# Kernel optimization log

Hardware: AMD Instinct MI355X
Metric: run time of the kernel (lower is better)

The kernel has to match this reference:

```python
import jax, jax.numpy as jnp
import numpy as np

LN_EPS = 1e-5

def _layernorm(z, g, b):
    m = jnp.mean(z, axis=-1, keepdims=True)
    v = jnp.mean(jnp.square(z - m), axis=-1, keepdims=True)
    return (z - m) / jnp.sqrt(v + LN_EPS) * g + b

def setup_inputs() -> dict:
    key = jax.random.key(0)
    ks = jax.random.split(key, 8)
    B, N, C, H = 16, 1024, 384, 6
    Dff = 4 * C
    s = 0.02
    return {
        "x": jax.random.normal(ks[0], (B, N, C), dtype=jnp.float32),
        "ln1_g": jnp.ones((C,), jnp.float32),
        "ln1_b": jnp.zeros((C,), jnp.float32),
        "qkv_w": jax.random.normal(ks[1], (3 * C, C), jnp.float32) * s,
        "proj_w": jax.random.normal(ks[2], (C, C), jnp.float32) * s,
        "proj_b": jnp.zeros((C,), jnp.float32),
        "gate_h": jnp.ones((H,), jnp.float32),
        "ln2_g": jnp.ones((C,), jnp.float32),
        "ln2_b": jnp.zeros((C,), jnp.float32),
        "fc1_w": jax.random.normal(ks[3], (Dff, C), jnp.float32) * s,
        "fc1_b": jnp.zeros((Dff,), jnp.float32),
        "fc2_w": jax.random.normal(ks[4], (C, Dff), jnp.float32) * s,
        "fc2_b": jnp.zeros((C,), jnp.float32),
        "gate_mlp": jnp.ones((Dff,), jnp.float32),
    }

def reference(x, ln1_g, ln1_b, qkv_w, proj_w, proj_b, gate_h,
              ln2_g, ln2_b, fc1_w, fc1_b, fc2_w, fc2_b, gate_mlp):
    B, N, C = x.shape
    H = gate_h.shape[0]
    Dh = C // H
    scale = Dh ** -0.5

    # Attention branch
    h = _layernorm(x, ln1_g, ln1_b)
    qkv = (h @ qkv_w.T).reshape(B, N, 3, H, Dh).transpose(2, 0, 3, 1, 4)  # [3,B,H,N,Dh]
    q, k, v = qkv[0], qkv[1], qkv[2]
    attn = jax.nn.softmax(jnp.einsum('bhnd,bhmd->bhnm', q, k) * scale, axis=-1)  # [B,H,N,N]
    o = jnp.einsum('bhnm,bhmd->bhnd', attn, v)            # [B,H,N,Dh]
    o = o.transpose(0, 2, 1, 3) * gate_h[None, None, :, None]  # per-head gate
    o = o.reshape(B, N, C) @ proj_w.T + proj_b
    x = x + o

    # MLP branch (exact GELU, per-neuron gate)
    h2 = _layernorm(x, ln2_g, ln2_b)
    m = jax.nn.gelu(h2 @ fc1_w.T + fc1_b, approximate=False) * gate_mlp
    x = x + (m @ fc2_w.T + fc2_b)
    return x
```

## Files before the change

kernel.cpp:

```cpp
#include <hip/hip_runtime.h>
#include <hip/hip_bf16.h>
#include <cstdint>
#include <cstddef>

#define B_   16
#define N_   1024
#define C_   384
#define H_   6
#define DFF_ 1536
#define R_   16384

typedef __attribute__((ext_vector_type(8))) __bf16 bf16x8;
typedef __attribute__((ext_vector_type(4))) float  f32x4;
typedef __attribute__((ext_vector_type(8))) unsigned short u16x8;
typedef __attribute__((ext_vector_type(4))) unsigned short u16x4;

__device__ __forceinline__ float bf2f(unsigned short u){
    unsigned int x = ((unsigned int)u) << 16;
    return __builtin_bit_cast(float, x);
}
__device__ __forceinline__ unsigned short f2bf(float f){
    return __builtin_bit_cast(unsigned short, __float2bfloat16(f));
}
__device__ __forceinline__ unsigned int cvt_pk_bf16(float a, float b){
    unsigned int r;
    asm("v_cvt_pk_bf16_f32 %0, %1, %2" : "=v"(r) : "v"(a), "v"(b));
    return r;
}
__device__ __forceinline__ float fast_exp2(float x){
    float r;
    asm("v_exp_f32 %0, %1" : "=v"(r) : "v"(x));
    return r;
}
__device__ __forceinline__ void gload16(const void* g, void* l){
    __builtin_amdgcn_global_load_lds(
        (const __attribute__((address_space(1))) unsigned int*)g,
        (__attribute__((address_space(3))) unsigned int*)l, 16, 0, 0);
}
__device__ __forceinline__ float gelu_f(float u){
    float z  = fabsf(u) * 0.70710678118654752f;
    float t  = __builtin_amdgcn_rcpf(1.0f + 0.47047f*z);
    float e  = __expf(-z*z);
    float p  = t*(0.3480242f + t*(-0.0958798f + t*0.7478556f));
    float er = 1.0f - p*e;
    return 0.5f*u*(1.0f + copysignf(er, u));
}
__device__ __forceinline__ float ldv(const float* p, size_t i){ return p[i]; }
__device__ __forceinline__ float ldv(const __hip_bfloat16* p, size_t i){ return __bfloat162float(p[i]); }

__global__ __launch_bounds__(256) void ln1_cvt_kernel(
    const float* __restrict__ x, const float* __restrict__ g,
    const float* __restrict__ b, __hip_bfloat16* __restrict__ out,
    const float* __restrict__ i0, __hip_bfloat16* __restrict__ o0, int n0,
    const float* __restrict__ i1, __hip_bfloat16* __restrict__ o1, int n1,
    const float* __restrict__ i2, __hip_bfloat16* __restrict__ o2, int n2,
    const float* __restrict__ i3, __hip_bfloat16* __restrict__ o3, int n3)
{
    if (blockIdx.x < 4096){
        const int lane = threadIdx.x & 63;
        const int wave = threadIdx.x >> 6;
        const int row  = blockIdx.x*4 + wave;
        const float* xr = x + (size_t)row*C_;
        float v[6];
        float s = 0.f;
        #pragma unroll
        for (int i=0;i<6;i++){ v[i] = xr[lane + i*64]; s += v[i]; }
        #pragma unroll
        for (int m=1;m<64;m<<=1) s += __shfl_xor(s, m);
        const float mean = s * (1.0f/C_);
        float sq = 0.f;
        #pragma unroll
        for (int i=0;i<6;i++){ float d = v[i]-mean; sq += d*d; }
        #pragma unroll
        for (int m=1;m<64;m<<=1) sq += __shfl_xor(sq, m);
        const float rstd = rsqrtf(sq*(1.0f/C_) + 1e-5f);
        #pragma unroll
        for (int i=0;i<6;i++){
            int c = lane + i*64;
            out[(size_t)row*C_ + c] = __float2bfloat16((v[i]-mean)*rstd*g[c] + b[c]);
        }
    } else {
        const int total = n0+n1+n2+n3;
        for (int i = (blockIdx.x-4096)*blockDim.x + threadIdx.x; i < total; i += 1024*blockDim.x){
            int k = i;
            if (k < n0){ o0[k] = __float2bfloat16(i0[k]); continue; }
            k -= n0;
            if (k < n1){ o1[k] = __float2bfloat16(i1[k]); continue; }
            k -= n1;
            if (k < n2){ o2[k] = __float2bfloat16(i2[k]); continue; }
            k -= n2;
            o3[k] = __float2bfloat16(i3[k]);
        }
    }
}

template<typename T>
__global__ __launch_bounds__(256) void ln_kernel(
    const T* __restrict__ x, const float* __restrict__ g,
    const float* __restrict__ b, __hip_bfloat16* __restrict__ out)
{
    const int lane = threadIdx.x & 63;
    const int wave = threadIdx.x >> 6;
    const int row  = blockIdx.x*4 + wave;
    const T* xr = x + (size_t)row*C_;
    float v[6];
    float s = 0.f;
    #pragma unroll
    for (int i=0;i<6;i++){ v[i] = ldv(xr, lane + i*64); s += v[i]; }
    #pragma unroll
    for (int m=1;m<64;m<<=1) s += __shfl_xor(s, m);
    const float mean = s * (1.0f/C_);
    float sq = 0.f;
    #pragma unroll
    for (int i=0;i<6;i++){ float d = v[i]-mean; sq += d*d; }
    #pragma unroll
    for (int m=1;m<64;m<<=1) sq += __shfl_xor(sq, m);
    const float rstd = rsqrtf(sq*(1.0f/C_) + 1e-5f);
    #pragma unroll
    for (int i=0;i<6;i++){
        int c = lane + i*64;
        out[(size_t)row*C_ + c] = __float2bfloat16((v[i]-mean)*rstd*g[c] + b[c]);
    }
}

#define BK2 32
enum { EPI_QKV=0, EPI_PROJ=1, EPI_FC1=2, EPI_FC2=3 };

template<int EPI, int BMt, int BNt, int NBUF, int MW, int NTH>
__global__ __launch_bounds__(NTH, MW) void gemm_bt(
    const __hip_bfloat16* __restrict__ A,
    const __hip_bfloat16* __restrict__ W,
    const int M, const int N, const int K,
    const float* __restrict__ bias,
    const float* __restrict__ resid,
    const __hip_bfloat16* __restrict__ residb,
    const float* __restrict__ gate,
    float* __restrict__ outf,
    __hip_bfloat16* __restrict__ outb)
{
    constexpr int NWAVE = NTH/64;
    constexpr int NWC   = (BNt >= 128) ? 2 : 1;
    constexpr int NWR   = NWAVE/NWC;
    constexpr int WRS   = BMt/NWR;
    constexpr int MI    = WRS/16;
    constexpr int APASS = (BMt*BK2*2)/(NTH*16);
    constexpr int BPASS = (BNt*BK2*2)/(NTH*16);
    constexpr int LPT   = APASS + BPASS;
    constexpr int RPP   = NTH/4;
    __shared__ __align__(16) unsigned short As[NBUF][BMt*BK2];
    __shared__ __align__(16) unsigned short Bs[NBUF][BNt*BK2];
    const int t = threadIdx.x;
    const int l = t & 63;
    const int w = t >> 6;
    const int wr = (NWC==2) ? (w >> 1) : w;
    const int wc = (NWC==2) ? (w & 1)  : 0;
    const int nb = N / BNt;
    const int rbX = (M/BMt) >> 3;
    const int X  = blockIdx.x & 7;
    const int j8 = blockIdx.x >> 3;
    const int rb = X*rbX + j8 / nb;
    const int cb = j8 % nb;
    const int srow2 = t >> 2;
    const int sgcol = (((t&3) - ((t>>3)&3)) & 3) * 8;
    f32x4 acc[MI][4];
    #pragma unroll
    for (int i=0;i<MI;i++)
        #pragma unroll
        for (int jj=0;jj<4;jj++) acc[i][jj] = (f32x4){0.f,0.f,0.f,0.f};

    const size_t arow0 = (size_t)rb*BMt + srow2;
    const size_t brow0 = (size_t)cb*BNt + srow2;

    auto STAGE = [&](int buf, int k0){
        #pragma unroll
        for (int c=0;c<APASS;c++)
            gload16(A + (arow0 + c*RPP)*K + k0 + sgcol, (char*)&As[buf][0] + c*(NTH*16) + t*16);
        #pragma unroll
        for (int c=0;c<BPASS;c++)
            gload16(W + (brow0 + c*RPP)*K + k0 + sgcol, (char*)&Bs[buf][0] + c*(NTH*16) + t*16);
    };

    auto COMPUTE = [&](int buf){
        const char* as = (const char*)&As[buf][0];
        const char* bs = (const char*)&Bs[buf][0];
        bf16x8 af[MI], bw[4];
        #pragma unroll
        for (int i=0;i<MI;i++){
            const int r = wr*WRS + i*16 + (l&15);
            const int sl = ((l>>4) + ((r>>1)&3)) & 3;
            af[i] = *(const bf16x8*)(as + r*64 + sl*16);
        }
        #pragma unroll
        for (int i=0;i<4;i++){
            const int r = wc*64 + i*16 + (l&15);
            const int sl = ((l>>4) + ((r>>1)&3)) & 3;
            bw[i] = *(const bf16x8*)(bs + r*64 + sl*16);
        }
        #pragma unroll
        for (int mi=0;mi<MI;mi++)
            #pragma unroll
            for (int ni=0;ni<4;ni++)
                acc[mi][ni] = __builtin_amdgcn_mfma_f32_16x16x32_bf16(af[mi], bw[ni], acc[mi][ni], 0,0,0);
    };

    const int nst = K/BK2;
    if constexpr (NBUF==2){
        STAGE(0, 0);
        for (int s=0; s<nst; ++s){
            asm volatile("s_waitcnt vmcnt(0)" ::: "memory");
            __builtin_amdgcn_s_barrier();
            asm volatile("" ::: "memory");
            if (s+1 < nst) STAGE((s+1)&1, (s+1)*BK2);
            COMPUTE(s&1);
        }
    } else {
        STAGE(0, 0);
        STAGE(1, BK2);
        int cur = 0, stb = 2;
        for (int s=0; s<nst; ++s){
            if (s < nst-1){
                if constexpr (LPT==4) asm volatile("s_waitcnt vmcnt(4)" ::: "memory");
                else                  asm volatile("s_waitcnt vmcnt(3)" ::: "memory");
            } else {
                asm volatile("s_waitcnt vmcnt(0)" ::: "memory");
            }
            __builtin_amdgcn_s_barrier();
            asm volatile("" ::: "memory");
            if (s+2 < nst){
                STAGE(stb, (s+2)*BK2);
                stb = (stb+1==3) ? 0 : stb+1;
            }
            COMPUTE(cur);
            cur = (cur+1==3) ? 0 : cur+1;
        }
    }
    const int rowBase = rb*BMt + wr*WRS;
    const int colBase = cb*BNt + wc*64;
    #pragma unroll
    for (int ni=0; ni<4; ni++){
        const int col = colBase + ni*16 + (l&15);
        #pragma unroll
        for (int mi=0; mi<MI; mi++){
            #pragma unroll
            for (int jj=0;jj<4;jj++){
                const int row = rowBase + mi*16 + (l>>4)*4 + jj;
                const float vx = acc[mi][ni][jj];
                size_t idx = (size_t)row*N + col;
                if constexpr (EPI==EPI_PROJ){
                    outb[idx] = __float2bfloat16(resid[idx] + vx + bias[col]);
                } else if constexpr (EPI==EPI_FC2){
                    outf[idx] = bf2f(*((const unsigned short*)residb + idx)) + vx + bias[col];
                } else {
                    outb[idx] = __float2bfloat16(gelu_f(vx + bias[col]) * gate[col]);
                }
            }
        }
    }
}

template<int EPI, int NCOLS>
__global__ __launch_bounds__(256, 2) void gemm_wres(
    const __hip_bfloat16* __restrict__ A,
    const __hip_bfloat16* __restrict__ Wt,
    const float* __restrict__ bias,
    const float* __restrict__ resid,
    const float* __restrict__ gate,
    __hip_bfloat16* __restrict__ outb)
{
    constexpr int NB = NCOLS/64;
    constexpr int G  = 24;
    __shared__ __align__(16) unsigned short As[4][128*32];
    __shared__ __align__(16) unsigned short Bs[64*384];
    const int t = threadIdx.x;
    const int l = t & 63;
    const int w = t >> 6;
    const int X  = blockIdx.x & 7;
    const int j8 = blockIdx.x >> 3;
    const int rb = X*8 + j8 / NB;
    const int cb = j8 % NB;

    #pragma unroll
    for (int j=0;j<12;j++){
        const int L     = (w*12 + j)*1024 + l*16;
        const int row   = L / 768;
        const int cbyte = L - row*768;
        const int scol  = (cbyte ^ ((row&7)<<4)) >> 1;
        gload16(Wt + (size_t)(cb*64 + row)*384 + scol, (char*)&Bs[0] + L);
    }
    const int sgcol = (((l&3) - ((l>>3)&3)) & 3) * 8;
    const size_t arow0 = (size_t)rb*256 + w*32 + (l>>2);
    auto STAGEA = [&](int g){
        const int rt = g/12, s = g - rt*12;
        #pragma unroll
        for (int c=0;c<2;c++)
            gload16(A + (arow0 + rt*128 + c*16)*384 + s*32 + sgcol,
                    (char*)&As[g&3][0] + w*2048 + c*1024 + l*16);
    };
    STAGEA(0); STAGEA(1); STAGEA(2);
    asm volatile("s_waitcnt vmcnt(6)" ::: "memory");
    __builtin_amdgcn_s_barrier();

    #pragma unroll
    for (int rt=0; rt<2; ++rt){
        f32x4 acc[2][4];
        #pragma unroll
        for (int i=0;i<2;i++)
            #pragma unroll
            for (int jj=0;jj<4;jj++) acc[i][jj] = (f32x4){0.f,0.f,0.f,0.f};

        #pragma unroll
        for (int s=0; s<12; ++s){
            const int g = rt*12 + s;
            if (g <= G-3)      asm volatile("s_waitcnt vmcnt(4)" ::: "memory");
            else if (g == G-2) asm volatile("s_waitcnt vmcnt(2)" ::: "memory");
            else               asm volatile("s_waitcnt vmcnt(0)" ::: "memory");
            const char* as = (const char*)&As[g&3][0] + w*2048;
            bf16x8 af[2], bw[4];
            #pragma unroll
            for (int i=0;i<2;i++){
                const int r  = i*16 + (l&15);
                const int sl = ((l>>4) + ((r>>1)&3)) & 3;
                af[i] = *(const bf16x8*)(as + r*64 + sl*16);
            }
            #pragma unroll
            for (int i=0;i<4;i++){
                const int r = i*16 + (l&15);
                bw[i] = *(const bf16x8*)((const char*)&Bs[0] + r*768
                             + ((s*64 + (l>>4)*16) ^ ((r&7)<<4)));
            }
            #pragma unroll
            for (int mi=0;mi<2;mi++)
                #pragma unroll
                for (int ni=0;ni<4;ni++)
                    acc[mi][ni] = __builtin_amdgcn_mfma_f32_16x16x32_bf16(af[mi], bw[ni], acc[mi][ni], 0,0,0);
            asm volatile("s_waitcnt lgkmcnt(0)" ::: "memory");
            if (g+3 < G) STAGEA(g+3);
        }
        const int rowBase = rb*256 + rt*128 + w*32;
        if constexpr (EPI==EPI_QKV){
            unsigned short* ob = (unsigned short*)outb;
            #pragma unroll
            for (int ni=0; ni<4; ni++){
                const int col = cb*64 + ni*16 + (l&15);
                const int p = col/384, rem = col - p*384;
                const int hh = rem>>6, d = rem&63;
                #pragma unroll
                for (int mi=0; mi<2; mi++){
                    const int row0 = rowBase + mi*16 + (l>>4)*4;
                    const int bb = row0>>10, n = row0&1023;
                    if (p==2){
                        u16x4 pk;
                        #pragma unroll
                        for (int jj=0;jj<4;jj++) pk[jj] = f2bf(acc[mi][ni][jj]);
                        *(u16x4*)(ob + (size_t)2*6291456 + ((size_t)(bb*H_+hh)*64 + d)*1024 + n) = pk;
                    } else {
                        #pragma unroll
                        for (int jj=0;jj<4;jj++)
                            ob[(((size_t)((p*16+bb)*6+hh))<<16) + ((size_t)(n+jj)<<6) + d] = f2bf(acc[mi][ni][jj]);
                    }
                }
            }
        } else {
            #pragma unroll
            for (int ni=0; ni<4; ni++){
                const int col = cb*64 + ni*16 + (l&15);
                #pragma unroll
                for (int mi=0; mi<2; mi++){
                    #pragma unroll
                    for (int jj=0;jj<4;jj++){
                        const int row = rowBase + mi*16 + (l>>4)*4 + jj;
                        const size_t idx = (size_t)row*NCOLS + col;
                        if constexpr (EPI==EPI_PROJ){
                            outb[idx] = __float2bfloat16(resid[idx] + acc[mi][ni][jj] + bias[col]);
                        } else {
                            outb[idx] = __float2bfloat16(gelu_f(acc[mi][ni][jj] + bias[col]) * gate[col]);
                        }
                    }
                }
            }
        }
    }
}

__global__ __launch_bounds__(256) void attn_mfma(
    const __hip_bfloat16* __restrict__ qg,
    const __hip_bfloat16* __restrict__ kg,
    const __hip_bfloat16* __restrict__ vtg,
    const float* __restrict__ gate_h,
    __hip_bfloat16* __restrict__ og)
{
    __shared__ __align__(16) unsigned short Ks [3][64*64];
    __shared__ __align__(16) unsigned short Vts[3][64*64];
    const int t = threadIdx.x;
    const int l = t & 63;
    const int w = t >> 6;
    const int X  = blockIdx.x & 7;
    const int j8 = blockIdx.x >> 3;
    const int bh = X*12 + (j8 >> 3);
    const int n0 = (j8 & 7) * 128;
    const int h  = bh % H_;
    const int b  = bh / H_;
    const unsigned short* qp  = (const unsigned short*)qg  + ((size_t)bh*N_ + n0 + w*32)*64;
    const unsigned short* kp  = (const unsigned short*)kg  + (size_t)bh*N_*64;
    const unsigned short* vtp = (const unsigned short*)vtg + (size_t)bh*64*N_;

    bf16x8 qf[2][2];
    #pragma unroll
    for (int mt=0;mt<2;mt++)
        #pragma unroll
        for (int dc=0;dc<2;dc++){
            u16x8 raw = *(const u16x8*)(qp + ((size_t)(mt*16 + (l&15)))*64 + dc*32 + (l>>4)*8);
            u16x8 sc;
            #pragma unroll
            for (int j=0;j<8;j++) sc[j] = f2bf(bf2f(raw[j]) * 0.1803368801111244f);
            qf[mt][dc] = __builtin_bit_cast(bf16x8, sc);
        }

    int qk_off[4][2], pv_off[2][4];
    #pragma unroll
    for (int t4=0;t4<4;t4++){
        const int i    = l & 15;
        const int row  = 8*(i>>2) + (i&3) + 4*(t4&1) + 32*(t4>>1);
        const int swzr = (row&3) | (((row>>3)&1)<<2);
        #pragma unroll
        for (int dc=0;dc<2;dc++)
            qk_off[t4][dc] = row*128 + ((dc*64 + (l>>4)*16) ^ (swzr<<4));
    }
    #pragma unroll
    for (int nt=0;nt<4;nt++){
        const int row  = nt*16 + (l&15);
        const int swzr = (row&3) | (((row>>3)&1)<<2);
        #pragma unroll
        for (int kc=0;kc<2;kc++)
            pv_off[kc][nt] = row*128 + ((kc*64 + (l>>4)*16) ^ (swzr<<4));
    }

    const int sr  = t >> 3;
    const int sce = (t & 7) * 8;

    auto STAGE = [&](int buf, int kt){
        #pragma unroll
        for (int c=0;c<2;c++){
            const int r    = sr + c*32;
            const int swzr = (r&3) | (((r>>3)&1)<<2);
            const int col  = sce ^ (swzr<<3);
            gload16(kp  + ((size_t)(kt*64 + r))*64 + col, (char*)&Ks [buf][0] + (c*256 + t)*16);
            gload16(vtp + (size_t)r*N_ + kt*64 + col,     (char*)&Vts[buf][0] + (c*256 + t)*16);
        }
    };

    f32x4 o_acc[2][4];
    #pragma unroll
    for (int i=0;i<2;i++)
        #pragma unroll
        for (int jj=0;jj<4;jj++) o_acc[i][jj] = (f32x4){0.f,0.f,0.f,0.f};
    float rs_part[2] = {0.f, 0.f};

    STAGE(0, 0);
    STAGE(1, 1);
    int cur = 0, stb = 2;
    for (int kt=0; kt<16; kt++){
        if (kt < 15) asm volatile("s_waitcnt vmcnt(4)" ::: "memory");
        else         asm volatile("s_waitcnt vmcnt(0)" ::: "memory");
        __builtin_amdgcn_s_barrier();
        asm volatile("" ::: "memory");
        if (kt < 14){
            STAGE(stb, kt+2);
            stb = (stb+1==3) ? 0 : stb+1;
        }
        const char* ks = (const char*)&Ks[cur][0];
        const char* vs = (const char*)&Vts[cur][0];

        f32x4 s_acc[4][2];
        #pragma unroll
        for (int i=0;i<4;i++)
            #pragma unroll
            for (int jj=0;jj<2;jj++) s_acc[i][jj] = (f32x4){0.f,0.f,0.f,0.f};
        #pragma unroll
        for (int t4=0;t4<4;t4++)
            #pragma unroll
            for (int dc=0;dc<2;dc++){
                bf16x8 kf = *(const bf16x8*)(ks + qk_off[t4][dc]);
                #pragma unroll
                for (int mt=0;mt<2;mt++)
                    s_acc[t4][mt] = __builtin_amdgcn_mfma_f32_16x16x32_bf16(kf, qf[mt][dc], s_acc[t4][mt], 0,0,0);
            }
        #pragma unroll
        for (int mt=0;mt<2;mt++){
            float acc_s = 0.f;
            #pragma unroll
            for (int t4=0;t4<4;t4++){
                #pragma unroll
                for (int jj=0;jj<4;jj++){
                    float e = fast_exp2(s_acc[t4][mt][jj]);
                    s_acc[t4][mt][jj] = e;
                    acc_s += e;
                }
            }
            rs_part[mt] += acc_s;
        }
        #pragma unroll
        for (int kc=0;kc<2;kc++){
            union { unsigned int u[4]; bf16x8 v; } pu[2];
            #pragma unroll
            for (int mt=0;mt<2;mt++){
                pu[mt].u[0] = cvt_pk_bf16(s_acc[2*kc  ][mt][0], s_acc[2*kc  ][mt][1]);
                pu[mt].u[1] = cvt_pk_bf16(s_acc[2*kc  ][mt][2], s_acc[2*kc  ][mt][3]);
                pu[mt].u[2] = cvt_pk_bf16(s_acc[2*kc+1][mt][0], s_acc[2*kc+1][mt][1]);
                pu[mt].u[3] = cvt_pk_bf16(s_acc[2*kc+1][mt][2], s_acc[2*kc+1][mt][3]);
            }
            #pragma unroll
            for (int nt=0;nt<4;nt++){
                bf16x8 vf = *(const bf16x8*)(vs + pv_off[kc][nt]);
                #pragma unroll
                for (int mt=0;mt<2;mt++)
                    o_acc[mt][nt] = __builtin_amdgcn_mfma_f32_16x16x32_bf16(pu[mt].v, vf, o_acc[mt][nt], 0,0,0);
            }
        }
        cur = (cur+1==3) ? 0 : cur+1;
    }
    float rowsum[2];
    #pragma unroll
    for (int mt=0;mt<2;mt++){
        float rs = rs_part[mt];
        rs += __shfl_xor(rs, 16);
        rs += __shfl_xor(rs, 32);
        rowsum[mt] = rs;
    }
    const float gh = gate_h[h];
    float inv[2][4];
    #pragma unroll
    for (int mt=0;mt<2;mt++)
        #pragma unroll
        for (int r=0;r<4;r++)
            inv[mt][r] = gh / __shfl(rowsum[mt], (l>>4)*4 + r, 16);
    unsigned short* op = (unsigned short*)og + ((size_t)b*N_ + n0 + w*32)*C_ + h*64;
    #pragma unroll
    for (int mt=0;mt<2;mt++){
        #pragma unroll
        for (int r=0;r<4;r++){
            const int n = mt*16 + (l>>4)*4 + r;
            #pragma unroll
            for (int nt=0;nt<4;nt++)
                op[(size_t)n*C_ + nt*16 + (l&15)] = f2bf(o_acc[mt][nt][r]*inv[mt][r]);
        }
    }
}

extern "C" void kernel_launch(void* const* d_in, const int* in_sizes, int n_in,
                              void* d_out, int out_size, void* d_ws, size_t ws_size,
                              hipStream_t stream)
{
    const float* x     = (const float*)d_in[0];
    const float* ln1g  = (const float*)d_in[1];
    const float* ln1b  = (const float*)d_in[2];
    const float* qkvw  = (const float*)d_in[3];
    const float* projw = (const float*)d_in[4];
    const float* projb = (const float*)d_in[5];
    const float* gateh = (const float*)d_in[6];
    const float* ln2g  = (const float*)d_in[7];
    const float* ln2b  = (const float*)d_in[8];
    const float* fc1w  = (const float*)d_in[9];
    const float* fc1b  = (const float*)d_in[10];
    const float* fc2w  = (const float*)d_in[11];
    const float* fc2b  = (const float*)d_in[12];
    const float* gatem = (const float*)d_in[13];
    float* out = (float*)d_out;

    char* ws = (char*)d_ws;
    __hip_bfloat16* h_buf = (__hip_bfloat16*)(ws + 0);
    __hip_bfloat16* qkv   = (__hip_bfloat16*)(ws + 12582912);
    __hip_bfloat16* q_buf = qkv;
    __hip_bfloat16* k_buf = qkv + 6291456;
    __hip_bfloat16* vt_buf= qkv + 2*6291456;
    __hip_bfloat16* o_buf = (__hip_bfloat16*)(ws + 50331648);
    __hip_bfloat16* m_buf = (__hip_bfloat16*)(ws + 12582912);
    __hip_bfloat16* x1b   = (__hip_bfloat16*)(ws + 62914560);
    __hip_bfloat16* wqkv  = (__hip_bfloat16*)(ws + 88080384);
    __hip_bfloat16* wproj = (__hip_bfloat16*)(ws + 88965120);
    __hip_bfloat16* wfc1  = (__hip_bfloat16*)(ws + 89260032);
    __hip_bfloat16* wfc2  = (__hip_bfloat16*)(ws + 90439680);

    ln1_cvt_kernel<<<5120, 256, 0, stream>>>(x, ln1g, ln1b, h_buf,
                                             qkvw, wqkv, 1152*384,
                                             projw, wproj, 384*384,
                                             fc1w, wfc1, 1536*384,
                                             fc2w, wfc2, 384*1536);

    gemm_wres<EPI_QKV,1152><<<1152, 256, 0, stream>>>(h_buf, wqkv, nullptr, nullptr, nullptr, qkv);
    attn_mfma<<<768, 256, 0, stream>>>(q_buf, k_buf, vt_buf, gateh, o_buf);
    gemm_wres<EPI_PROJ,384><<<384, 256, 0, stream>>>(o_buf, wproj, projb, x, nullptr, x1b);
    ln_kernel<__hip_bfloat16><<<4096, 256, 0, stream>>>(x1b, ln2g, ln2b, h_buf);
    gemm_wres<EPI_FC1,1536><<<1536, 256, 0, stream>>>(h_buf, wfc1, fc1b, nullptr, gatem, m_buf);
    gemm_bt<EPI_FC2,64,128,3,1,256><<<768, 256, 0, stream>>>(m_buf, wfc2, R_, 384, 1536,
                                                             fc2b, nullptr, x1b, nullptr, out, nullptr);
}
```

Before: 171.0 us.

## Load GEMM A operand directly into registers, halve row tile, raise occupancy

Replaces the LDS-staged, multi-buffered A-tile pipeline in the weight-resident GEMM with direct global-to-register loads of A fragments, prefetched three k-steps ahead. Each block now handles 128 rows instead of 256, so the grid doubles, LDS drops to the weight tile only, and launch bounds allow three blocks per CU. This removes the A staging through shared memory and its waitcnt choreography. In exchange, the weight tile is loaded into LDS twice as often across the grid, and A fragments come from uncoalesced-per-lane global loads whose latency is hidden only by register prefetch and occupancy.

Result: slower. 193.5 us (+13.1%).

```diff
diff --git a/kernel.cpp b/kernel.cpp
--- a/kernel.cpp
+++ b/kernel.cpp
@@ -259,7 +259,7 @@
 }
 
 template<int EPI, int NCOLS>
-__global__ __launch_bounds__(256, 2) void gemm_wres(
+__global__ __launch_bounds__(256, 3) void gemm_areg(
     const __hip_bfloat16* __restrict__ A,
     const __hip_bfloat16* __restrict__ Wt,
     const float* __restrict__ bias,
@@ -268,15 +268,13 @@
     __hip_bfloat16* __restrict__ outb)
 {
     constexpr int NB = NCOLS/64;
-    constexpr int G  = 24;
-    __shared__ __align__(16) unsigned short As[4][128*32];
     __shared__ __align__(16) unsigned short Bs[64*384];
     const int t = threadIdx.x;
     const int l = t & 63;
     const int w = t >> 6;
     const int X  = blockIdx.x & 7;
     const int j8 = blockIdx.x >> 3;
-    const int rb = X*8 + j8 / NB;
+    const int rb = X*16 + j8 / NB;
     const int cb = j8 % NB;
 
     #pragma unroll
@@ -287,94 +285,84 @@
         const int scol  = (cbyte ^ ((row&7)<<4)) >> 1;
         gload16(Wt + (size_t)(cb*64 + row)*384 + scol, (char*)&Bs[0] + L);
     }
-    const int sgcol = (((l&3) - ((l>>3)&3)) & 3) * 8;
-    const size_t arow0 = (size_t)rb*256 + w*32 + (l>>2);
-    auto STAGEA = [&](int g){
-        const int rt = g/12, s = g - rt*12;
-        #pragma unroll
-        for (int c=0;c<2;c++)
-            gload16(A + (arow0 + rt*128 + c*16)*384 + s*32 + sgcol,
-                    (char*)&As[g&3][0] + w*2048 + c*1024 + l*16);
-    };
-    STAGEA(0); STAGEA(1); STAGEA(2);
-    asm volatile("s_waitcnt vmcnt(6)" ::: "memory");
+
+    const unsigned short* Ap = (const unsigned short*)A
+        + ((size_t)rb*128 + w*32 + (l&15))*384 + (l>>4)*8;
+    bf16x8 af[3][2];
+    #pragma unroll
+    for (int p=0;p<3;p++)
+        #pragma unroll
+        for (int i=0;i<2;i++)
+            af[p][i] = *(const bf16x8*)(Ap + (size_t)i*16*384 + p*32);
+
+    asm volatile("s_waitcnt vmcnt(0)" ::: "memory");
     __builtin_amdgcn_s_barrier();
 
-    #pragma unroll
-    for (int rt=0; rt<2; ++rt){
-        f32x4 acc[2][4];
-        #pragma unroll
-        for (int i=0;i<2;i++)
-            #pragma unroll
-            for (int jj=0;jj<4;jj++) acc[i][jj] = (f32x4){0.f,0.f,0.f,0.f};
-
-        #pragma unroll
-        for (int s=0; s<12; ++s){
-            const int g = rt*12 + s;
-            if (g <= G-3)      asm volatile("s_waitcnt vmcnt(4)" ::: "memory");
-            else if (g == G-2) asm volatile("s_waitcnt vmcnt(2)" ::: "memory");
-            else               asm volatile("s_waitcnt vmcnt(0)" ::: "memory");
-            const char* as = (const char*)&As[g&3][0] + w*2048;
-            bf16x8 af[2], bw[4];
-            #pragma unroll
-            for (int i=0;i<2;i++){
-                const int r  = i*16 + (l&15);
-                const int sl = ((l>>4) + ((r>>1)&3)) & 3;
-                af[i] = *(const bf16x8*)(as + r*64 + sl*16);
-            }
-            #pragma unroll
-            for (int i=0;i<4;i++){
-                const int r = i*16 + (l&15);
-                bw[i] = *(const bf16x8*)((const char*)&Bs[0] + r*768
-                             + ((s*64 + (l>>4)*16) ^ ((r&7)<<4)));
-            }
-            #pragma unroll
-            for (int mi=0;mi<2;mi++)
+    f32x4 acc[2][4];
+    #pragma unroll
+    for (int i=0;i<2;i++)
+        #pragma unroll
+        for (int jj=0;jj<4;jj++) acc[i][jj] = (f32x4){0.f,0.f,0.f,0.f};
+
+    #pragma unroll
+    for (int s=0; s<12; ++s){
+        bf16x8 bw[4];
+        #pragma unroll
+        for (int i=0;i<4;i++){
+            const int r = i*16 + (l&15);
+            bw[i] = *(const bf16x8*)((const char*)&Bs[0] + r*768
+                         + ((s*64 + (l>>4)*16) ^ ((r&7)<<4)));
+        }
+        #pragma unroll
+        for (int ni=0;ni<4;ni++){
+            acc[0][ni] = __builtin_amdgcn_mfma_f32_16x16x32_bf16(af[s%3][0], bw[ni], acc[0][ni], 0,0,0);
+            acc[1][ni] = __builtin_amdgcn_mfma_f32_16x16x32_bf16(af[s%3][1], bw[ni], acc[1][ni], 0,0,0);
+        }
+        if (s+3 < 12){
+            #pragma unroll
+            for (int i=0;i<2;i++)
+                af[(s+3)%3][i] = *(const bf16x8*)(Ap + (size_t)i*16*384 + (s+3)*32);
+        }
+    }
+
+    const int rowBase = rb*128 + w*32;
+    if constexpr (EPI==EPI_QKV){
+        unsigned short* ob = (unsigned short*)outb;
+        #pragma unroll
+        for (int ni=0; ni<4; ni++){
+            const int col = cb*64 + ni*16 + (l&15);
+            const int p = col/384, rem = col - p*384;
+            const int hh = rem>>6, d = rem&63;
+            #pragma unroll
+            for (int mi=0; mi<2; mi++){
+                const int row0 = rowBase + mi*16 + (l>>4)*4;
+                const int bb = row0>>10, n = row0&1023;
+                if (p==2){
+                    u16x4 pk;
+                    #pragma unroll
+                    for (int jj=0;jj<4;jj++) pk[jj] = f2bf(acc[mi][ni][jj]);
+                    *(u16x4*)(ob + (size_t)2*6291456 + ((size_t)(bb*H_+hh)*64 + d)*1024 + n) = pk;
+                } else {
+                    #pragma unroll
+                    for (int jj=0;jj<4;jj++)
+                        ob[(((size_t)((p*16+bb)*6+hh))<<16) + ((size_t)(n+jj)<<6) + d] = f2bf(acc[mi][ni][jj]);
+                }
+            }
+        }
+    } else {
+        #pragma unroll
+        for (int ni=0; ni<4; ni++){
+            const int col = cb*64 + ni*16 + (l&15);
+            #pragma unroll
+            for (int mi=0; mi<2; mi++){
                 #pragma unroll
-                for (int ni=0;ni<4;ni++)
-                    acc[mi][ni] = __builtin_amdgcn_mfma_f32_16x16x32_bf16(af[mi], bw[ni], acc[mi][ni], 0,0,0);
-            asm volatile("s_waitcnt lgkmcnt(0)" ::: "memory");
-            if (g+3 < G) STAGEA(g+3);
-        }
-        const int rowBase = rb*256 + rt*128 + w*32;
-        if constexpr (EPI==EPI_QKV){
-            unsigned short* ob = (unsigned short*)outb;
-            #pragma unroll
-            for (int ni=0; ni<4; ni++){
-                const int col = cb*64 + ni*16 + (l&15);
-                const int p = col/384, rem = col - p*384;
-                const int hh = rem>>6, d = rem&63;
-                #pragma unroll
-                for (int mi=0; mi<2; mi++){
-                    const int row0 = rowBase + mi*16 + (l>>4)*4;
-                    const int bb = row0>>10, n = row0&1023;
-                    if (p==2){
-                        u16x4 pk;
-                        #pragma unroll
-                        for (int jj=0;jj<4;jj++) pk[jj] = f2bf(acc[mi][ni][jj]);
-                        *(u16x4*)(ob + (size_t)2*6291456 + ((size_t)(bb*H_+hh)*64 + d)*1024 + n) = pk;
+                for (int jj=0;jj<4;jj++){
+                    const int row = rowBase + mi*16 + (l>>4)*4 + jj;
+                    const size_t idx = (size_t)row*NCOLS + col;
+                    if constexpr (EPI==EPI_PROJ){
+                        outb[idx] = __float2bfloat16(resid[idx] + acc[mi][ni][jj] + bias[col]);
                     } else {
-                        #pragma unroll
-                        for (int jj=0;jj<4;jj++)
-                            ob[(((size_t)((p*16+bb)*6+hh))<<16) + ((size_t)(n+jj)<<6) + d] = f2bf(acc[mi][ni][jj]);
-                    }
-                }
-            }
-        } else {
-            #pragma unroll
-            for (int ni=0; ni<4; ni++){
-                const int col = cb*64 + ni*16 + (l&15);
-                #pragma unroll
-                for (int mi=0; mi<2; mi++){
-                    #pragma unroll
-                    for (int jj=0;jj<4;jj++){
-                        const int row = rowBase + mi*16 + (l>>4)*4 + jj;
-                        const size_t idx = (size_t)row*NCOLS + col;
-                        if constexpr (EPI==EPI_PROJ){
-                            outb[idx] = __float2bfloat16(resid[idx] + acc[mi][ni][jj] + bias[col]);
-                        } else {
-                            outb[idx] = __float2bfloat16(gelu_f(acc[mi][ni][jj] + bias[col]) * gate[col]);
-                        }
+                        outb[idx] = __float2bfloat16(gelu_f(acc[mi][ni][jj] + bias[col]) * gate[col]);
                     }
                 }
             }
@@ -587,11 +575,11 @@
                                              fc1w, wfc1, 1536*384,
                                              fc2w, wfc2, 384*1536);
 
-    gemm_wres<EPI_QKV,1152><<<1152, 256, 0, stream>>>(h_buf, wqkv, nullptr, nullptr, nullptr, qkv);
+    gemm_areg<EPI_QKV,1152><<<2304, 256, 0, stream>>>(h_buf, wqkv, nullptr, nullptr, nullptr, qkv);
     attn_mfma<<<768, 256, 0, stream>>>(q_buf, k_buf, vt_buf, gateh, o_buf);
-    gemm_wres<EPI_PROJ,384><<<384, 256, 0, stream>>>(o_buf, wproj, projb, x, nullptr, x1b);
+    gemm_areg<EPI_PROJ,384><<<768, 256, 0, stream>>>(o_buf, wproj, projb, x, nullptr, x1b);
     ln_kernel<__hip_bfloat16><<<4096, 256, 0, stream>>>(x1b, ln2g, ln2b, h_buf);
-    gemm_wres<EPI_FC1,1536><<<1536, 256, 0, stream>>>(h_buf, wfc1, fc1b, nullptr, gatem, m_buf);
+    gemm_areg<EPI_FC1,1536><<<3072, 256, 0, stream>>>(h_buf, wfc1, fc1b, nullptr, gatem, m_buf);
     gemm_bt<EPI_FC2,64,128,3,1,256><<<768, 256, 0, stream>>>(m_buf, wfc2, R_, 384, 1536,
                                                              fc2b, nullptr, x1b, nullptr, out, nullptr);
 }
```

## Add 128-row weight-resident GEMM variant for FC1 with 4-stage A pipeline

Applied to the files above, without the earlier changes.

Adds a new gemm_wres4 kernel in which each block keeps a 64-column weight slice resident in LDS and computes a single 128x64 output tile. A-tiles stream through a 4-deep async buffer, with explicit vmcnt waits and a swizzled LDS layout. FC1 now launches this kernel with 3072 blocks instead of 1536, giving finer-grained work and better load balance. The cost is reloading the weight slice twice as often per output.

Result: no change. 173.7 us (+1.6%).

```diff
diff --git a/kernel.cpp b/kernel.cpp
--- a/kernel.cpp
+++ b/kernel.cpp
@@ -258,6 +258,7 @@
     }
 }
 
+
 template<int EPI, int NCOLS>
 __global__ __launch_bounds__(256, 2) void gemm_wres(
     const __hip_bfloat16* __restrict__ A,
@@ -376,6 +377,100 @@
                             outb[idx] = __float2bfloat16(gelu_f(acc[mi][ni][jj] + bias[col]) * gate[col]);
                         }
                     }
+                }
+            }
+        }
+    }
+}
+
+template<int EPI, int NCOLS>
+__global__ __launch_bounds__(256, 2) void gemm_wres4(
+    const __hip_bfloat16* __restrict__ A,
+    const __hip_bfloat16* __restrict__ Wt,
+    const float* __restrict__ bias,
+    const float* __restrict__ resid,
+    const float* __restrict__ gate,
+    __hip_bfloat16* __restrict__ outb)
+{
+    constexpr int NB = NCOLS/64;
+    __shared__ __align__(16) unsigned short As[4][128*32];
+    __shared__ __align__(16) unsigned short Bs[64*384];
+    const int t = threadIdx.x;
+    const int l = t & 63;
+    const int w = t >> 6;
+    const int X  = blockIdx.x & 7;
+    const int j8 = blockIdx.x >> 3;
+    const int rb = X*16 + j8 / NB;
+    const int cb = j8 % NB;
+
+    #pragma unroll
+    for (int j=0;j<12;j++){
+        const int L     = (w*12 + j)*1024 + l*16;
+        const int row   = L / 768;
+        const int cbyte = L - row*768;
+        const int scol  = (cbyte ^ ((row&7)<<4)) >> 1;
+        gload16(Wt + (size_t)(cb*64 + row)*384 + scol, (char*)&Bs[0] + L);
+    }
+    const int sgcol = (((l&3) - ((l>>3)&3)) & 3) * 8;
+    const size_t arow0 = (size_t)rb*128 + w*32 + (l>>2);
+    auto STAGEA = [&](int g){
+        #pragma unroll
+        for (int c=0;c<2;c++)
+            gload16(A + (arow0 + c*16)*384 + g*32 + sgcol,
+                    (char*)&As[g&3][0] + w*2048 + c*1024 + l*16);
+    };
+    STAGEA(0); STAGEA(1); STAGEA(2);
+    asm volatile("s_waitcnt vmcnt(6)" ::: "memory");
+    __builtin_amdgcn_s_barrier();
+
+    f32x4 acc[2][4];
+    #pragma unroll
+    for (int i=0;i<2;i++)
+        #pragma unroll
+        for (int jj=0;jj<4;jj++) acc[i][jj] = (f32x4){0.f,0.f,0.f,0.f};
+
+    #pragma unroll
+    for (int s=0; s<12; ++s){
+        if (s < 10)      asm volatile("s_waitcnt vmcnt(4)" ::: "memory");
+        else if (s == 10) asm volatile("s_waitcnt vmcnt(2)" ::: "memory");
+        else              asm volatile("s_waitcnt vmcnt(0)" ::: "memory");
+        const char* as = (const char*)&As[s&3][0] + w*2048;
+        bf16x8 af[2], bw[4];
+        #pragma unroll
+        for (int i=0;i<2;i++){
+            const int r  = i*16 + (l&15);
+            const int sl = ((l>>4) + ((r>>1)&3)) & 3;
+            af[i] = *(const bf16x8*)(as + r*64 + sl*16);
+        }
+        #pragma unroll
+        for (int i=0;i<4;i++){
+            const int r = i*16 + (l&15);
+            bw[i] = *(const bf16x8*)((const char*)&Bs[0] + r*768
+                         + ((s*64 + (l>>4)*16) ^ ((r&7)<<4)));
+        }
+        #pragma unroll
+        for (int mi=0;mi<2;mi++)
+            #pragma unroll
+            for (int ni=0;ni<4;ni++)
+                acc[mi][ni] = __builtin_amdgcn_mfma_f32_16x16x32_bf16(af[mi], bw[ni], acc[mi][ni], 0,0,0);
+        asm volatile("s_waitcnt lgkmcnt(0)" ::: "memory");
+        if (s+3 < 12) STAGEA(s+3);
+    }
+
+    const int rowBase = rb*128 + w*32;
+    #pragma unroll
+    for (int ni=0; ni<4; ni++){
+        const int col = cb*64 + ni*16 + (l&15);
+        #pragma unroll
+        for (int mi=0; mi<2; mi++){
+            #pragma unroll
+            for (int jj=0;jj<4;jj++){
+                const int row = rowBase + mi*16 + (l>>4)*4 + jj;
+                const size_t idx = (size_t)row*NCOLS + col;
+                if constexpr (EPI==EPI_PROJ){
+                    outb[idx] = __float2bfloat16(resid[idx] + acc[mi][ni][jj] + bias[col]);
+                } else {
+                    outb[idx] = __float2bfloat16(gelu_f(acc[mi][ni][jj] + bias[col]) * gate[col]);
                 }
             }
         }
@@ -591,7 +686,7 @@
     attn_mfma<<<768, 256, 0, stream>>>(q_buf, k_buf, vt_buf, gateh, o_buf);
     gemm_wres<EPI_PROJ,384><<<384, 256, 0, stream>>>(o_buf, wproj, projb, x, nullptr, x1b);
     ln_kernel<__hip_bfloat16><<<4096, 256, 0, stream>>>(x1b, ln2g, ln2b, h_buf);
-    gemm_wres<EPI_FC1,1536><<<1536, 256, 0, stream>>>(h_buf, wfc1, fc1b, nullptr, gatem, m_buf);
+    gemm_wres4<EPI_FC1,1536><<<3072, 256, 0, stream>>>(h_buf, wfc1, fc1b, nullptr, gatem, m_buf);
     gemm_bt<EPI_FC2,64,128,3,1,256><<<768, 256, 0, stream>>>(m_buf, wfc2, R_, 384, 1536,
                                                              fc2b, nullptr, x1b, nullptr, out, nullptr);
 }
```
